# Optimization experiments

Hardware: AMD Instinct MI355X
Metric: run time of the kernel (lower is better)

Reference implementation:

```python
import jax, jax.numpy as jnp
import numpy as np

B, S, H, R = 2, 4096, 2048, 2048
NB, CW = 16, 4
BW = R // NB


def _block_diag_linear(x, w, b):
    # x: [B,S,R]; w: [NB,BW,BW]; b: [NB,BW]
    xb = x.reshape(x.shape[0], x.shape[1], NB, BW)
    out = jnp.einsum('bsni,nij->bsnj', xb, w) + b
    return out.reshape(x.shape)


def _causal_conv1d(x, conv_w, conv_b):
    # depthwise causal temporal conv: out[t] = sum_i w[i]*x[t-CW+1+i] + b
    xp = jnp.pad(x, ((0, 0), (CW - 1, 0), (0, 0)))
    out = conv_b
    for i in range(CW):
        out = out + conv_w[i] * xp[:, i:i + x.shape[1], :]
    return out


def _rg_lru_scan(x, x_gate_pre, a_gate_pre, a_param):
    gate_x = jax.nn.sigmoid(x_gate_pre)
    gate_a = jax.nn.sigmoid(a_gate_pre)
    log_a = -8.0 * gate_a * jax.nn.softplus(a_param)  # [B,S,R]
    a = jnp.exp(log_a)
    multiplier = jnp.sqrt(-jnp.expm1(2.0 * log_a))  # sqrt(1 - a^2)
    norm_x = x * gate_x * multiplier
    # h_t = a_t * h_{t-1} + norm_x_t via parallel associative scan over time
    def combine(c1, c2):
        a1, b1 = c1
        a2, b2 = c2
        return a1 * a2, a2 * b1 + b2
    _, h = jax.lax.associative_scan(combine, (a, norm_x), axis=1)
    return h


def setup_inputs() -> dict:
    key = jax.random.key(0)
    ks = jax.random.split(key, 9)
    x = jax.random.normal(ks[0], (B, S, H), dtype=jnp.float32)
    W_xy = jax.random.normal(ks[1], (2 * R, H), dtype=jnp.float32) / np.sqrt(H)
    ig_w = jax.random.normal(ks[2], (NB, BW, BW), dtype=jnp.float32) / np.sqrt(BW)
    ig_b = jnp.zeros((NB, BW), dtype=jnp.float32)
    ag_w = jax.random.normal(ks[3], (NB, BW, BW), dtype=jnp.float32) / np.sqrt(BW)
    ag_b = jnp.zeros((NB, BW), dtype=jnp.float32)
    # forget_init: a = a_real in [0.9, 0.999]; a_param = softplus^{-1}(-log(a_real))
    unif = jax.random.uniform(ks[4], (R,), dtype=jnp.float32)
    a_real = 0.5 * jnp.log(unif * (0.999 ** 2 - 0.9 ** 2) + 0.9 ** 2 + 1e-8)
    a_param = jnp.log(jnp.expm1(-a_real))
    conv_w = jax.random.normal(ks[5], (CW, R), dtype=jnp.float32) / np.sqrt(CW * R)
    conv_b = jnp.zeros((R,), dtype=jnp.float32)
    # resid_proj is zero-init in the module; use small random so output is non-trivial
    W_resid = 0.02 * jax.random.normal(ks[6], (H, R), dtype=jnp.float32)
    return {"x": x, "W_xy": W_xy, "ig_w": ig_w, "ig_b": ig_b,
            "ag_w": ag_w, "ag_b": ag_b, "a_param": a_param,
            "conv_w": conv_w, "conv_b": conv_b, "W_resid": W_resid}


def reference(x, W_xy, ig_w, ig_b, ag_w, ag_b, a_param, conv_w, conv_b, W_resid):
    xy = jnp.einsum('bsh,rh->bsr', x, W_xy)  # [B,S,2R]
    xr, y = jnp.split(xy, 2, axis=-1)
    xc = _causal_conv1d(xr, conv_w, conv_b)
    x_gate_pre = _block_diag_linear(xc, ig_w, ig_b)
    a_gate_pre = _block_diag_linear(xc, ag_w, ag_b)
    h = _rg_lru_scan(xc, x_gate_pre, a_gate_pre, a_param)
    out = jnp.einsum('bsr,hr->bsh', jax.nn.gelu(y, approximate=False) * h, W_resid)
    return out
```

## Files before the change

kernel.cpp:

```cpp
#include <hip/hip_runtime.h>
#include <hip/hip_bf16.h>

typedef __hip_bfloat16 bf16;
typedef __attribute__((ext_vector_type(8))) short s16x8;
typedef __attribute__((ext_vector_type(4))) float f32x4;

#define B_ 2
#define S_ 4096
#define H_ 2048
#define R_ 2048
#define M_ 8192
#define NB_ 16
#define BW_ 128
#define CHUNK 64
#define NCH 64

__device__ __forceinline__ short f2b_s(float f) {
    return (short)__builtin_bit_cast(unsigned short, __float2bfloat16(f));
}
__device__ __forceinline__ float b2f_s(short s) {
    unsigned int u = ((unsigned int)(unsigned short)s) << 16;
    return __builtin_bit_cast(float, u);
}
__device__ __forceinline__ float sigm_fast(float x) { return 1.f / (1.f + __expf(-x)); }

__device__ __forceinline__ void async_g2l(const void* g, void* l) {
    __builtin_amdgcn_global_load_lds((const __attribute__((address_space(1))) void*)g,
                                     (__attribute__((address_space(3))) void*)l, 16, 0, 0);
}

__global__ __launch_bounds__(256) void cast_f32_bf16(const float* __restrict__ in,
                                                     bf16* __restrict__ out, int n) {
    int idx = blockIdx.x * 256 + threadIdx.x;
    int i8 = idx * 8;
    if (i8 >= n) return;
    float4 v0 = *(const float4*)(in + i8);
    float4 v1 = *(const float4*)(in + i8 + 4);
    s16x8 o;
    o[0] = f2b_s(v0.x); o[1] = f2b_s(v0.y); o[2] = f2b_s(v0.z); o[3] = f2b_s(v0.w);
    o[4] = f2b_s(v1.x); o[5] = f2b_s(v1.y); o[6] = f2b_s(v1.z); o[7] = f2b_s(v1.w);
    *(s16x8*)(out + i8) = o;
}

__global__ __launch_bounds__(256) void wcast_T(const float* __restrict__ igw,
                                               const float* __restrict__ agw,
                                               bf16* __restrict__ wT) {
    int idx = blockIdx.x * 256 + threadIdx.x;
    int p = idx >> 18;
    int rem = idx & 262143;
    int n = rem >> 14;
    int ji = rem & 16383;
    int j = ji >> 7, i = ji & 127;
    const float* w = p ? agw : igw;
    wT[idx] = __float2bfloat16(w[(n << 14) + (i << 7) + j]);
}

__global__ __launch_bounds__(256) void sp8_kernel(const float* __restrict__ apar,
                                                  float* __restrict__ sp8) {
    int r = blockIdx.x * 256 + threadIdx.x;
    float ap = apar[r];
    sp8[r] = 8.f * (ap > 20.f ? ap : log1pf(expf(ap)));
}

__device__ __forceinline__ void store_c(float* p, float v) { *p = v; }
__device__ __forceinline__ void store_c(bf16* p, float v) { *p = __float2bfloat16(v); }

template <typename OutT>
__global__ __launch_bounds__(256, 4) void gemm_bt(const bf16* __restrict__ A,
                                                  const bf16* __restrict__ Bm,
                                                  OutT* __restrict__ C,
                                                  int K, int lda, int ldb, int ldc) {
    __shared__ __align__(16) short As[128 * 64];
    __shared__ __align__(16) short Bs[128 * 64];
    const int tid = threadIdx.x;
    const int lane = tid & 63, wave = tid >> 6;
    const int waveM = wave >> 1, waveN = wave & 1;
    const int mBase = blockIdx.y * 128, nBase = blockIdx.x * 128;
    const int fm = lane & 15, q = lane >> 4;

    f32x4 acc[4][4];
#pragma unroll
    for (int i = 0; i < 4; ++i)
#pragma unroll
        for (int j = 0; j < 4; ++j) acc[i][j] = (f32x4){0.f, 0.f, 0.f, 0.f};

    for (int k0 = 0; k0 < K; k0 += 64) {
        __syncthreads();
#pragma unroll
        for (int it = 0; it < 4; ++it) {
            int off = it * 4096 + tid * 16;
            int r = off >> 7;
            int g = ((off & 127) >> 4) ^ (r & 7);
            async_g2l(A + (size_t)(mBase + r) * lda + k0 + g * 8, (char*)As + off);
            async_g2l(Bm + (size_t)(nBase + r) * ldb + k0 + g * 8, (char*)Bs + off);
        }
        __syncthreads();
#pragma unroll
        for (int s = 0; s < 2; ++s) {
            s16x8 af[4], bfr[4];
#pragma unroll
            for (int i = 0; i < 4; ++i) {
                int row = waveM * 64 + i * 16 + fm;
                af[i] = *(const s16x8*)((char*)As + row * 128 + ((((s << 2) + q) ^ (row & 7)) << 4));
                int col = waveN * 64 + i * 16 + fm;
                bfr[i] = *(const s16x8*)((char*)Bs + col * 128 + ((((s << 2) + q) ^ (col & 7)) << 4));
            }
#pragma unroll
            for (int i = 0; i < 4; ++i)
#pragma unroll
                for (int j = 0; j < 4; ++j)
                    acc[i][j] = __builtin_amdgcn_mfma_f32_16x16x32_bf16(af[i], bfr[j], acc[i][j], 0, 0, 0);
        }
    }
#pragma unroll
    for (int i = 0; i < 4; ++i) {
        int rowg = mBase + waveM * 64 + i * 16 + q * 4;
#pragma unroll
        for (int j = 0; j < 4; ++j) {
            int colg = nBase + waveN * 64 + j * 16 + fm;
#pragma unroll
            for (int rr = 0; rr < 4; ++rr)
                store_c(C + (size_t)(rowg + rr) * ldc + colg, acc[i][j][rr]);
        }
    }
}

__global__ __launch_bounds__(256) void conv_kernel(const bf16* __restrict__ xy,
                                                   const float* __restrict__ cw,
                                                   const float* __restrict__ cb,
                                                   bf16* __restrict__ xc) {
    int idx = blockIdx.x * 256 + threadIdx.x;
    int r = idx & (R_ - 1);
    int m = idx >> 11;
    int t = m & (S_ - 1);
    float v = cb[r];
    const bf16* base = xy + (size_t)m * 4096 + r;
#pragma unroll
    for (int i = 0; i < 4; ++i) {
        int tt = t - 3 + i;
        if (tt >= 0) v += cw[i * R_ + r] * __bfloat162float(base[(ptrdiff_t)(i - 3) * 4096]);
    }
    xc[idx] = __float2bfloat16(v);
}

__global__ __launch_bounds__(256) void gate_kernel(const bf16* __restrict__ xc,
                                                   const bf16* __restrict__ wT,
                                                   const float* __restrict__ igb,
                                                   const float* __restrict__ agb,
                                                   const float* __restrict__ sp8,
                                                   bf16* __restrict__ la_out,
                                                   bf16* __restrict__ nx_out,
                                                   float* __restrict__ Ach,
                                                   float* __restrict__ Hla) {
    __shared__ __align__(16) short As[64 * 128];
    __shared__ __align__(16) char  Wmem[128 * 256];
    short* Ws = (short*)Wmem;
    float* a_sh = (float*)Wmem;
    const int n = blockIdx.x;
    const int mBase = blockIdx.y * 64;
    const int tid = threadIdx.x;
    const int lane = tid & 63, wave = tid >> 6;
    const int fm = lane & 15, q = lane >> 4;

#pragma unroll
    for (int it = 0; it < 4; ++it) {
        int off = it * 4096 + tid * 16;
        int r = off >> 8;
        int g = ((off & 255) >> 4) ^ (r & 15);
        async_g2l(xc + (size_t)(mBase + r) * R_ + n * BW_ + g * 8, (char*)As + off);
    }
    const bf16* w0 = wT + (size_t)n * 16384;
#pragma unroll
    for (int it = 0; it < 8; ++it) {
        int off = it * 4096 + tid * 16;
        int j = off >> 8;
        int g = ((off & 255) >> 4) ^ (j & 15);
        async_g2l(w0 + j * 128 + g * 8, (char*)Ws + off);
    }
    __syncthreads();

    f32x4 accI[8], accA[8];
#pragma unroll
    for (int jj = 0; jj < 8; ++jj) {
        accI[jj] = (f32x4){0.f, 0.f, 0.f, 0.f};
        accA[jj] = (f32x4){0.f, 0.f, 0.f, 0.f};
    }

    const int row = wave * 16 + fm;
#pragma unroll
    for (int s = 0; s < 4; ++s) {
        s16x8 af = *(const s16x8*)((char*)As + row * 256 + ((((s << 2) + q) ^ (row & 15)) << 4));
#pragma unroll
        for (int jj = 0; jj < 8; ++jj) {
            int wrow = jj * 16 + fm;
            s16x8 bw = *(const s16x8*)((char*)Ws + wrow * 256 + ((((s << 2) + q) ^ (wrow & 15)) << 4));
            accI[jj] = __builtin_amdgcn_mfma_f32_16x16x32_bf16(af, bw, accI[jj], 0, 0, 0);
        }
    }
    __syncthreads();
    const bf16* w1 = wT + (size_t)(NB_ + n) * 16384;
#pragma unroll
    for (int it = 0; it < 8; ++it) {
        int off = it * 4096 + tid * 16;
        int j = off >> 8;
        int g = ((off & 255) >> 4) ^ (j & 15);
        async_g2l(w1 + j * 128 + g * 8, (char*)Ws + off);
    }
    __syncthreads();
#pragma unroll
    for (int s = 0; s < 4; ++s) {
        s16x8 af = *(const s16x8*)((char*)As + row * 256 + ((((s << 2) + q) ^ (row & 15)) << 4));
#pragma unroll
        for (int jj = 0; jj < 8; ++jj) {
            int wrow = jj * 16 + fm;
            s16x8 bw = *(const s16x8*)((char*)Ws + wrow * 256 + ((((s << 2) + q) ^ (wrow & 15)) << 4));
            accA[jj] = __builtin_amdgcn_mfma_f32_16x16x32_bf16(af, bw, accA[jj], 0, 0, 0);
        }
    }
    __syncthreads();

#pragma unroll
    for (int jj = 0; jj < 8; ++jj) {
        int col = jj * 16 + fm;
        int r = n * BW_ + col;
        float bi = igb[r], ba = agb[r];
        float s8 = sp8[r];
#pragma unroll
        for (int rr = 0; rr < 4; ++rr) {
            int rowl = wave * 16 + q * 4 + rr;
            short* slot = (short*)((char*)As + rowl * 256 +
                          ((((col >> 3)) ^ (rowl & 15)) << 4) + (col & 7) * 2);
            float xcv = b2f_s(*slot);
            float xg = accI[jj][rr] + bi;
            float ag = accA[jj][rr] + ba;
            float la = -s8 * sigm_fast(ag);
            float av = __expf(la);
            float t2 = 2.f * la;
            float nem = (t2 > -0.125f)
                ? -t2 * (1.f + t2 * (0.5f + t2 * (0.16666667f + t2 * 0.04166667f)))
                : 1.f - av * av;
            float nxv = xcv * sigm_fast(xg) * sqrtf(nem);
            short nxs = f2b_s(nxv);
            size_t o = (size_t)(mBase + rowl) * R_ + r;
            la_out[o] = __float2bfloat16(la);
            nx_out[o] = __builtin_bit_cast(bf16, (unsigned short)nxs);
            a_sh[rowl * 128 + col] = av;
            *slot = nxs;
        }
    }
    __syncthreads();

    if (tid < 128) {
        int col = tid;
        float h = 0.f, cum = 1.f;
#pragma unroll 4
        for (int t = 0; t < CHUNK; ++t) {
            float a = a_sh[t * 128 + col];
            float nxv = b2f_s(*(const short*)((char*)As + t * 256 +
                              ((((col >> 3)) ^ (t & 15)) << 4) + (col & 7) * 2));
            h = fmaf(a, h, nxv);
            cum *= a;
        }
        int b = mBase >> 12, c = (mBase & (S_ - 1)) >> 6;
        int so = ((b * NCH + c) << 11) + n * BW_ + col;
        Ach[so] = cum;
        Hla[so] = h;
    }
}

__global__ __launch_bounds__(256) void scan_carry(const float* __restrict__ Ach,
                                                  const float* __restrict__ Hla,
                                                  float* __restrict__ carry) {
    int idx = blockIdx.x * 256 + threadIdx.x;
    int r = idx & (R_ - 1), b = idx >> 11;
    float cy = 0.f;
    for (int c = 0; c < NCH; ++c) {
        int o = (b * NCH + c) * R_ + r;
        carry[o] = cy;
        cy = fmaf(Ach[o], cy, Hla[o]);
    }
}

__global__ __launch_bounds__(256) void scan_passB(const bf16* __restrict__ la_buf,
                                                  const bf16* __restrict__ nx_buf,
                                                  const float* __restrict__ carry,
                                                  const bf16* __restrict__ xy,
                                                  bf16* __restrict__ g_out) {
    int bid = blockIdx.x;
    int rt = bid & 7, c = (bid >> 3) & 63, b = bid >> 9;
    int r = rt * 256 + threadIdx.x;
    int m0 = b * S_ + c * CHUNK;
    size_t base = (size_t)m0 * R_ + r;
    const bf16* yp = xy + (size_t)m0 * 4096 + 2048 + r;
    int so = (b * NCH + c) * R_ + r;
    float h = carry[so];
    for (int t = 0; t < CHUNK; ++t) {
        size_t o = base + (size_t)t * R_;
        float a = __expf(__bfloat162float(la_buf[o]));
        float nx = __bfloat162float(nx_buf[o]);
        h = fmaf(a, h, nx);
        float y = __bfloat162float(yp[(size_t)t * 4096]);
        float g = 0.5f * y * (1.f + erff(y * 0.70710678f));
        g_out[o] = __float2bfloat16(g * h);
    }
}

extern "C" void kernel_launch(void* const* d_in, const int* in_sizes, int n_in,
                              void* d_out, int out_size, void* d_ws, size_t ws_size,
                              hipStream_t stream) {
    const float* x    = (const float*)d_in[0];
    const float* Wxy  = (const float*)d_in[1];
    const float* igw  = (const float*)d_in[2];
    const float* igb  = (const float*)d_in[3];
    const float* agw  = (const float*)d_in[4];
    const float* agb  = (const float*)d_in[5];
    const float* apar = (const float*)d_in[6];
    const float* cw   = (const float*)d_in[7];
    const float* cb   = (const float*)d_in[8];
    const float* Wres = (const float*)d_in[9];
    float* out = (float*)d_out;

    char* ws = (char*)d_ws;
    const size_t MiB = (size_t)1 << 20;
    bf16*  xbf   = (bf16*)(ws);
    bf16*  la    = (bf16*)(ws);
    bf16*  wxyb  = (bf16*)(ws + 32 * MiB);
    bf16*  wT    = (bf16*)(ws + 32 * MiB);
    float* sp8   = (float*)(ws + 33 * MiB + 65536);
    bf16*  xy    = (bf16*)(ws + 48 * MiB);
    bf16*  wresb = (bf16*)(ws + 112 * MiB);
    bf16*  xc    = (bf16*)(ws + 120 * MiB);
    bf16*  g     = xc;
    bf16*  nx    = (bf16*)(ws + 152 * MiB);
    float* Ach   = (float*)(ws + 184 * MiB);
    float* Hla   = (float*)(ws + 185 * MiB);
    float* cyb   = (float*)(ws + 186 * MiB);

    cast_f32_bf16<<<8192, 256, 0, stream>>>(x, xbf, M_ * H_);
    cast_f32_bf16<<<4096, 256, 0, stream>>>(Wxy, wxyb, 2 * R_ * H_);
    cast_f32_bf16<<<2048, 256, 0, stream>>>(Wres, wresb, H_ * R_);

    gemm_bt<bf16><<<dim3(32, 64), 256, 0, stream>>>(xbf, wxyb, xy, 2048, 2048, 2048, 4096);

    conv_kernel<<<65536, 256, 0, stream>>>(xy, cw, cb, xc);

    wcast_T<<<2048, 256, 0, stream>>>(igw, agw, wT);
    sp8_kernel<<<8, 256, 0, stream>>>(apar, sp8);

    gate_kernel<<<dim3(NB_, 128), 256, 0, stream>>>(xc, wT, igb, agb, sp8, la, nx, Ach, Hla);

    scan_carry<<<16, 256, 0, stream>>>(Ach, Hla, cyb);
    scan_passB<<<1024, 256, 0, stream>>>(la, nx, cyb, xy, g);

    gemm_bt<float><<<dim3(16, 64), 256, 0, stream>>>(g, wresb, out, 2048, 2048, 2048, 2048);
}
```

Baseline: 501.4 us.

## Fuse causal conv into gate kernel, merge cast kernels, tile weight transpose

```diff
diff --git a/kernel.cpp b/kernel.cpp
--- a/kernel.cpp
+++ b/kernel.cpp
@@ -29,11 +29,18 @@
                                      (__attribute__((address_space(3))) void*)l, 16, 0, 0);
 }
 
-__global__ __launch_bounds__(256) void cast_f32_bf16(const float* __restrict__ in,
-                                                     bf16* __restrict__ out, int n) {
+__global__ __launch_bounds__(256) void cast_all(const float* __restrict__ x,
+                                                const float* __restrict__ wxy,
+                                                const float* __restrict__ wres,
+                                                bf16* __restrict__ xbf,
+                                                bf16* __restrict__ wxyb,
+                                                bf16* __restrict__ wresb) {
     int idx = blockIdx.x * 256 + threadIdx.x;
-    int i8 = idx * 8;
-    if (i8 >= n) return;
+    const float* in; bf16* out; int off;
+    if (idx < 2097152)      { in = x;    out = xbf;   off = idx; }
+    else if (idx < 3145728) { in = wxy;  out = wxyb;  off = idx - 2097152; }
+    else                    { in = wres; out = wresb; off = idx - 3145728; }
+    size_t i8 = (size_t)off * 8;
     float4 v0 = *(const float4*)(in + i8);
     float4 v1 = *(const float4*)(in + i8 + 4);
     s16x8 o;
@@ -45,14 +52,23 @@
 __global__ __launch_bounds__(256) void wcast_T(const float* __restrict__ igw,
                                                const float* __restrict__ agw,
                                                bf16* __restrict__ wT) {
-    int idx = blockIdx.x * 256 + threadIdx.x;
-    int p = idx >> 18;
-    int rem = idx & 262143;
-    int n = rem >> 14;
-    int ji = rem & 16383;
-    int j = ji >> 7, i = ji & 127;
-    const float* w = p ? agw : igw;
-    wT[idx] = __float2bfloat16(w[(n << 14) + (i << 7) + j]);
+    __shared__ float tile[128 * 129];
+    int blk = blockIdx.x;
+    int p = blk >> 4, n = blk & 15;
+    const float* w = (p ? agw : igw) + (size_t)n * 16384;
+    int tid = threadIdx.x;
+#pragma unroll
+    for (int it = 0; it < 64; ++it) {
+        int u = it * 256 + tid;
+        tile[(u >> 7) * 129 + (u & 127)] = w[u];
+    }
+    __syncthreads();
+    bf16* o = wT + (size_t)blk * 16384;
+#pragma unroll
+    for (int it = 0; it < 64; ++it) {
+        int u = it * 256 + tid;
+        o[u] = __float2bfloat16(tile[(u & 127) * 129 + (u >> 7)]);
+    }
 }
 
 __global__ __launch_bounds__(256) void sp8_kernel(const float* __restrict__ apar,
@@ -66,7 +82,7 @@
 __device__ __forceinline__ void store_c(bf16* p, float v) { *p = __float2bfloat16(v); }
 
 template <typename OutT>
-__global__ __launch_bounds__(256, 4) void gemm_bt(const bf16* __restrict__ A,
+__global__ __launch_bounds__(256, 5) void gemm_bt(const bf16* __restrict__ A,
                                                   const bf16* __restrict__ Bm,
                                                   OutT* __restrict__ C,
                                                   int K, int lda, int ldb, int ldc) {
@@ -125,25 +141,9 @@
     }
 }
 
-__global__ __launch_bounds__(256) void conv_kernel(const bf16* __restrict__ xy,
+__global__ __launch_bounds__(256) void gate_kernel(const bf16* __restrict__ xy,
                                                    const float* __restrict__ cw,
                                                    const float* __restrict__ cb,
-                                                   bf16* __restrict__ xc) {
-    int idx = blockIdx.x * 256 + threadIdx.x;
-    int r = idx & (R_ - 1);
-    int m = idx >> 11;
-    int t = m & (S_ - 1);
-    float v = cb[r];
-    const bf16* base = xy + (size_t)m * 4096 + r;
-#pragma unroll
-    for (int i = 0; i < 4; ++i) {
-        int tt = t - 3 + i;
-        if (tt >= 0) v += cw[i * R_ + r] * __bfloat162float(base[(ptrdiff_t)(i - 3) * 4096]);
-    }
-    xc[idx] = __float2bfloat16(v);
-}
-
-__global__ __launch_bounds__(256) void gate_kernel(const bf16* __restrict__ xc,
                                                    const bf16* __restrict__ wT,
                                                    const float* __restrict__ igb,
                                                    const float* __restrict__ agb,
@@ -154,21 +154,53 @@
                                                    float* __restrict__ Hla) {
     __shared__ __align__(16) short As[64 * 128];
     __shared__ __align__(16) char  Wmem[128 * 256];
-    short* Ws = (short*)Wmem;
+    short* Xs   = (short*)Wmem;
+    short* Ws   = (short*)Wmem;
     float* a_sh = (float*)Wmem;
     const int n = blockIdx.x;
     const int mBase = blockIdx.y * 64;
     const int tid = threadIdx.x;
     const int lane = tid & 63, wave = tid >> 6;
     const int fm = lane & 15, q = lane >> 4;
-
-#pragma unroll
-    for (int it = 0; it < 4; ++it) {
-        int off = it * 4096 + tid * 16;
-        int r = off >> 8;
-        int g = ((off & 255) >> 4) ^ (r & 15);
-        async_g2l(xc + (size_t)(mBase + r) * R_ + n * BW_ + g * 8, (char*)As + off);
-    }
+    const int t0 = mBase & (S_ - 1);
+
+#pragma unroll
+    for (int it = 0; it < 5; ++it) {
+        int u = it * 256 + tid;
+        if (u < 67 * 16) {
+            int rr = u >> 4, gg = u & 15;
+            s16x8 v = (s16x8){0, 0, 0, 0, 0, 0, 0, 0};
+            if (t0 != 0 || rr >= 3) {
+                int m = mBase + rr - 3;
+                v = *(const s16x8*)(xy + (size_t)m * 4096 + n * BW_ + gg * 8);
+            }
+            *(s16x8*)((char*)Xs + u * 16) = v;
+        }
+    }
+    __syncthreads();
+
+    {
+        int col = tid & 127, rh = tid >> 7;
+        int rbase = n * BW_ + col;
+        float w0c = cw[rbase], w1c = cw[R_ + rbase], w2c = cw[2 * R_ + rbase],
+              w3c = cw[3 * R_ + rbase];
+        float bc = cb[rbase];
+        int r0 = rh * 32;
+        float xm3 = b2f_s(Xs[(r0 + 0) * 128 + col]);
+        float xm2 = b2f_s(Xs[(r0 + 1) * 128 + col]);
+        float xm1 = b2f_s(Xs[(r0 + 2) * 128 + col]);
+#pragma unroll
+        for (int rw = 0; rw < 32; ++rw) {
+            int row = r0 + rw;
+            float x0 = b2f_s(Xs[(row + 3) * 128 + col]);
+            float v = bc + w0c * xm3 + w1c * xm2 + w2c * xm1 + w3c * x0;
+            xm3 = xm2; xm2 = xm1; xm1 = x0;
+            *(short*)((char*)As + row * 256 + ((((col >> 3)) ^ (row & 15)) << 4) +
+                      (col & 7) * 2) = f2b_s(v);
+        }
+    }
+    __syncthreads();
+
     const bf16* w0 = wT + (size_t)n * 16384;
 #pragma unroll
     for (int it = 0; it < 8; ++it) {
@@ -329,25 +361,21 @@
     float* sp8   = (float*)(ws + 33 * MiB + 65536);
     bf16*  xy    = (bf16*)(ws + 48 * MiB);
     bf16*  wresb = (bf16*)(ws + 112 * MiB);
-    bf16*  xc    = (bf16*)(ws + 120 * MiB);
-    bf16*  g     = xc;
+    bf16*  g     = (bf16*)(ws + 120 * MiB);
     bf16*  nx    = (bf16*)(ws + 152 * MiB);
     float* Ach   = (float*)(ws + 184 * MiB);
     float* Hla   = (float*)(ws + 185 * MiB);
     float* cyb   = (float*)(ws + 186 * MiB);
 
-    cast_f32_bf16<<<8192, 256, 0, stream>>>(x, xbf, M_ * H_);
-    cast_f32_bf16<<<4096, 256, 0, stream>>>(Wxy, wxyb, 2 * R_ * H_);
-    cast_f32_bf16<<<2048, 256, 0, stream>>>(Wres, wresb, H_ * R_);
+    cast_all<<<14336, 256, 0, stream>>>(x, Wxy, Wres, xbf, wxyb, wresb);
 
     gemm_bt<bf16><<<dim3(32, 64), 256, 0, stream>>>(xbf, wxyb, xy, 2048, 2048, 2048, 4096);
 
-    conv_kernel<<<65536, 256, 0, stream>>>(xy, cw, cb, xc);
-
-    wcast_T<<<2048, 256, 0, stream>>>(igw, agw, wT);
+    wcast_T<<<32, 256, 0, stream>>>(igw, agw, wT);
     sp8_kernel<<<8, 256, 0, stream>>>(apar, sp8);
 
-    gate_kernel<<<dim3(NB_, 128), 256, 0, stream>>>(xc, wT, igb, agb, sp8, la, nx, Ach, Hla);
+    gate_kernel<<<dim3(NB_, 128), 256, 0, stream>>>(xy, cw, cb, wT, igb, agb, sp8,
+                                                    la, nx, Ach, Hla);
 
     scan_carry<<<16, 256, 0, stream>>>(Ach, Hla, cyb);
     scan_passB<<<1024, 256, 0, stream>>>(la, nx, cyb, xy, g);
```

After: 558.4 us. 11.4% more time.
